# Kernel optimization log

Measured on AMD Instinct MI355X. Metric: run time of the kernel, lower is better.

The kernel has to match this reference:

```python
import jax, jax.numpy as jnp
import numpy as np

EPS = 1e-5

def _conv(x, w, b=None):
    # NCHW conv, stride 1, padding 1 (SAME for 3x3)
    y = jax.lax.conv_general_dilated(x, w, window_strides=(1, 1),
                                     padding=((1, 1), (1, 1)),
                                     dimension_numbers=('NCHW', 'OIHW', 'NCHW'))
    if b is not None:
        y = y + b[None, :, None, None]
    return y


def setup_inputs() -> dict:
    key = jax.random.key(0)
    ks = jax.random.split(key, 8)
    B, H, W = 4, 512, 640
    depth = jax.random.uniform(ks[0], (B, 1, H, W), dtype=jnp.float32) * 100.0
    img_feature = jax.random.normal(ks[1], (B, 16, H, W), dtype=jnp.float32)
    w1 = jax.random.normal(ks[2], (32, 16, 3, 3), dtype=jnp.float32) * 0.05
    b1 = jax.random.normal(ks[3], (32,), dtype=jnp.float32) * 0.05
    gamma = jnp.ones((32,), dtype=jnp.float32)
    beta = jnp.zeros((32,), dtype=jnp.float32)
    rmean = jax.random.normal(ks[4], (32,), dtype=jnp.float32) * 0.05
    rvar = jax.random.uniform(ks[5], (32,), dtype=jnp.float32) + 0.5
    w2 = jax.random.normal(ks[6], (9, 32, 3, 3), dtype=jnp.float32) * 0.05
    return {"depth": depth, "img_feature": img_feature, "w1": w1, "b1": b1,
            "gamma": gamma, "beta": beta, "rmean": rmean, "rvar": rvar, "w2": w2}


def reference(depth, img_feature, w1, b1, gamma, beta, rmean, rvar, w2):
    B, _, H, W = depth.shape
    # depth_propagation_layer: conv -> BN (eval, running stats) -> relu -> conv
    h1 = _conv(img_feature, w1, b1)
    h1 = (h1 - rmean[None, :, None, None]) * (gamma[None, :, None, None]
          * jax.lax.rsqrt(rvar + EPS)[None, :, None, None]) + beta[None, :, None, None]
    h1 = jax.nn.relu(h1)
    logits = _conv(h1, w2)                    # [B, 9, H, W]
    prob = jax.nn.softmax(logits, axis=1)     # per-pixel 3x3 filter weights
    dp = jnp.pad(depth, ((0, 0), (0, 0), (1, 1), (1, 1)), mode='edge')  # [B,1,H+2,W+2]
    patches = jnp.concatenate([dp[:, :, i:i + H, j:j + W]
                               for i in range(3) for j in range(3)], axis=1)  # [B,9,H,W]
    result_depth = jnp.sum(patches * prob, axis=1)  # [B, H, W]
    return result_depth
```

## Files before the change

kernel.cpp:

```cpp
#include <hip/hip_runtime.h>
#include <hip/hip_bf16.h>

#define HH 512
#define WW 640
#define HW (HH*WW)
#define NT 256

typedef short short8  __attribute__((ext_vector_type(8)));
typedef short short4v __attribute__((ext_vector_type(4)));
typedef float f32x16  __attribute__((ext_vector_type(16)));
typedef float f32x4   __attribute__((ext_vector_type(4)));

__device__ inline short f2bf(float f) {
    __hip_bfloat16 h = __float2bfloat16(f);
    short s; __builtin_memcpy(&s, &h, 2);
    return s;
}

__global__ void prep_weights(const float* __restrict__ w1, const float* __restrict__ b1,
                             const float* __restrict__ gamma, const float* __restrict__ beta,
                             const float* __restrict__ rmean, const float* __restrict__ rvar,
                             const float* __restrict__ w2,
                             short* __restrict__ ws_w1, short* __restrict__ ws_w2)
{
    int tid = blockIdx.x*blockDim.x + threadIdx.x;
    int stride = gridDim.x*blockDim.x;
    for (int i = tid; i < 4608; i += stride) {
        int oc = i / 144, rem = i - oc*144, c = rem / 9, t = rem - c*9;
        float a = gamma[oc] * rsqrtf(rvar[oc] + 1e-5f);
        ws_w1[t*512 + oc*16 + c] = f2bf(w1[i] * a);
    }
    for (int i = tid; i < 512; i += stride) {
        int oc = i >> 4, c = i & 15;
        float a = gamma[oc] * rsqrtf(rvar[oc] + 1e-5f);
        float bias = beta[oc] + (b1[oc] - rmean[oc]) * a;
        ws_w1[9*512 + i] = (c == 0) ? f2bf(bias) : (short)0;
    }
    for (int i = tid; i < 4608; i += stride) {
        int t = i >> 9, f = (i >> 5) & 15, c = i & 31;
        float val = (f < 9) ? w2[(f*32 + c)*9 + t] : 0.f;
        ws_w2[i] = f2bf(val);
    }
}

__launch_bounds__(NT, 4)
__global__ void fastprop_main(const float* __restrict__ depth,
                              const float* __restrict__ img,
                              const short* __restrict__ ws_w1,
                              const short* __restrict__ ws_w2,
                              float* __restrict__ out)
{
    __shared__ short s_img[468*16];
    __shared__ short s_h1 [360*32];
    __shared__ float s_depth[340];

    const int tid = threadIdx.x;

    int nid = blockIdx.x;
    int oid = (nid & 7)*640 + (nid >> 3);
    int bz = oid / 1280; int rem = oid - bz*1280;
    int by = rem / 20;   int bx = rem - by*20;
    const int gy0 = by*8, gx0 = bx*32;

    const float* imgb = img   + (size_t)bz*16*HW;
    const float* dpb  = depth + (size_t)bz*HW;

    const int lane = tid & 63;
    const int wid  = tid >> 6;

    const int oc = lane & 31, cg = lane >> 5;
    short8 a1[10];
    #pragma unroll
    for (int t = 0; t < 10; ++t)
        a1[t] = *(const short8*)&ws_w1[t*512 + oc*16 + cg*8];
    short8 bb = (short8)0;
    bb[0] = (cg == 0) ? (short)0x3F80 : (short)0;

    #pragma unroll
    for (int it = 0; it < 2; ++it) {
        int idx = tid + it*NT;
        if (idx < 468) {
            int iy = idx / 36, ix = idx - iy*36;
            int gy = gy0 + iy - 2, gx = gx0 + ix - 2;
            bool v = ((unsigned)gy < HH) && ((unsigned)gx < WW);
            int cy = min(max(gy, 0), HH-1), cx = min(max(gx, 0), WW-1);
            const float* p = imgb + cy*WW + cx;
            float m = v ? 1.f : 0.f;
            short8 v0, v1;
            #pragma unroll
            for (int c = 0; c < 8; ++c)  v0[c] = f2bf(m * p[c*HW]);
            #pragma unroll
            for (int c = 0; c < 8; ++c)  v1[c] = f2bf(m * p[(c+8)*HW]);
            *(short8*)&s_img[idx*16]     = v0;
            *(short8*)&s_img[idx*16 + 8] = v1;
        }
    }
    #pragma unroll
    for (int it = 0; it < 2; ++it) {
        int idx = tid + it*NT;
        if (idx < 340) {
            int ty = idx / 34, tx = idx - ty*34;
            int gy = min(max(gy0 + ty - 1, 0), HH-1);
            int gx = min(max(gx0 + tx - 1, 0), WW-1);
            s_depth[idx] = dpb[gy*WW + gx];
        }
    }
    __syncthreads();

    {
        const int OFS1[9] = {0, 16, 32, 576, 592, 608, 1152, 1168, 1184};

        #pragma unroll
        for (int gi = 0; gi < 3; ++gi) {
            int g    = wid + gi*4;
            int hp   = g*32 + (lane & 31);
            int base = hp*16 + cg*8;
            f32x16 acc;
            #pragma unroll
            for (int i = 0; i < 16; ++i) acc[i] = 0.f;
            acc = __builtin_amdgcn_mfma_f32_32x32x16_bf16(a1[9], bb, acc, 0, 0, 0);
            #pragma unroll
            for (int t = 0; t < 9; ++t)
                acc = __builtin_amdgcn_mfma_f32_32x32x16_bf16(
                         a1[t], *(const short8*)&s_img[base + OFS1[t]], acc, 0, 0, 0);

            if (hp < 360) {
                unsigned hy = (unsigned)hp / 36u;
                int hx = hp - (int)hy*36;
                int gy = gy0 + (int)hy - 1, gx = gx0 + hx - 1;
                bool inb = ((unsigned)gy < HH) && ((unsigned)gx < WW);
                #pragma unroll
                for (int q = 0; q < 4; ++q) {
                    short4v h;
                    #pragma unroll
                    for (int j = 0; j < 4; ++j) {
                        float hv = fmaxf(acc[q*4 + j], 0.f);
                        h[j] = inb ? f2bf(hv) : (short)0;
                    }
                    *(short4v*)&s_h1[hp*32 + 8*q + 4*cg] = h;
                }
            }
        }
    }
    __syncthreads();

    {
        const int fl = lane & 15, cg2 = lane >> 4;
        short8 a2[9];
        #pragma unroll
        for (int t = 0; t < 9; ++t)
            a2[t] = *(const short8*)&ws_w2[t*512 + fl*32 + cg2*8];

        const int OFS2[9] = {-1184, -1152, -1120, -32, 0, 32, 1120, 1152, 1184};

        #pragma unroll
        for (int gi = 0; gi < 4; ++gi) {
            int g  = wid + gi*4;
            int po = g*16 + fl;
            int oy = po >> 5, ox = po & 31;
            int hbase = ((oy + 1)*36 + (ox + 1))*32 + cg2*8;
            f32x4 acc;
            #pragma unroll
            for (int i = 0; i < 4; ++i) acc[i] = 0.f;
            #pragma unroll
            for (int t = 0; t < 9; ++t)
                acc = __builtin_amdgcn_mfma_f32_16x16x32_bf16(
                         a2[t], *(const short8*)&s_h1[hbase + OFS2[t]], acc, 0, 0, 0);

            float num = 0.f, den = 0.f;
            #pragma unroll
            for (int r = 0; r < 4; ++r) {
                int f = cg2*4 + r;
                if (f < 9) {
                    float e = __expf(acc[r]);
                    int fy = f/3, fx = f - fy*3;
                    float d = s_depth[(oy + fy)*34 + (ox + fx)];
                    den += e; num += e * d;
                }
            }
            num += __shfl_xor(num, 16); den += __shfl_xor(den, 16);
            num += __shfl_xor(num, 32); den += __shfl_xor(den, 32);
            if (cg2 == 0)
                out[(size_t)bz*HW + (size_t)(gy0 + oy)*WW + (gx0 + ox)] = num / den;
        }
    }
}

extern "C" void kernel_launch(void* const* d_in, const int* in_sizes, int n_in,
                              void* d_out, int out_size, void* d_ws, size_t ws_size,
                              hipStream_t stream) {
    const float* depth = (const float*)d_in[0];
    const float* img   = (const float*)d_in[1];
    const float* w1    = (const float*)d_in[2];
    const float* b1    = (const float*)d_in[3];
    const float* gamma = (const float*)d_in[4];
    const float* beta  = (const float*)d_in[5];
    const float* rmean = (const float*)d_in[6];
    const float* rvar  = (const float*)d_in[7];
    const float* w2    = (const float*)d_in[8];
    float* out = (float*)d_out;

    short* ws_w1 = (short*)d_ws;
    short* ws_w2 = ws_w1 + 5120;

    prep_weights<<<16, NT, 0, stream>>>(w1, b1, gamma, beta, rmean, rvar, w2,
                                        ws_w1, ws_w2);
    fastprop_main<<<5120, NT, 0, stream>>>(depth, img, ws_w1, ws_w2, out);
}
```

Before: 64.05 us.

## Switch LDS tiles to channel-planar layout and reuse h1 rows across output rows

Shared-memory image and h1 tiles move from pixel-interleaved to channel-group planar layout with padded planes, aiming to cut LDS bank conflicts on the MFMA operand loads. The image staging loop is split into half-channel work items so each thread issues fewer loads per iteration. In the second conv, each wave now handles two adjacent output rows and loads four h1 rows once into registers, feeding both accumulators and cutting redundant LDS reads. This raises register pressure per wave, which could hurt occupancy.

```diff
diff --git a/kernel.cpp b/kernel.cpp
--- a/kernel.cpp
+++ b/kernel.cpp
@@ -5,6 +5,8 @@
 #define WW 640
 #define HW (HH*WW)
 #define NT 256
+#define IMPLANEP (468*8 + 8)
+#define H1PLANEP (360*8 + 8)
 
 typedef short short8  __attribute__((ext_vector_type(8)));
 typedef short short4v __attribute__((ext_vector_type(4)));
@@ -50,8 +52,8 @@
                               const short* __restrict__ ws_w2,
                               float* __restrict__ out)
 {
-    __shared__ short s_img[468*16];
-    __shared__ short s_h1 [360*32];
+    __shared__ short s_img[2*IMPLANEP];
+    __shared__ short s_h1 [4*H1PLANEP];
     __shared__ float s_depth[340];
 
     const int tid = threadIdx.x;
@@ -76,24 +78,18 @@
     short8 bb = (short8)0;
     bb[0] = (cg == 0) ? (short)0x3F80 : (short)0;
 
-    #pragma unroll
-    for (int it = 0; it < 2; ++it) {
-        int idx = tid + it*NT;
-        if (idx < 468) {
-            int iy = idx / 36, ix = idx - iy*36;
-            int gy = gy0 + iy - 2, gx = gx0 + ix - 2;
-            bool v = ((unsigned)gy < HH) && ((unsigned)gx < WW);
-            int cy = min(max(gy, 0), HH-1), cx = min(max(gx, 0), WW-1);
-            const float* p = imgb + cy*WW + cx;
-            float m = v ? 1.f : 0.f;
-            short8 v0, v1;
-            #pragma unroll
-            for (int c = 0; c < 8; ++c)  v0[c] = f2bf(m * p[c*HW]);
-            #pragma unroll
-            for (int c = 0; c < 8; ++c)  v1[c] = f2bf(m * p[(c+8)*HW]);
-            *(short8*)&s_img[idx*16]     = v0;
-            *(short8*)&s_img[idx*16 + 8] = v1;
-        }
+    for (int g = tid; g < 936; g += NT) {
+        int pixel = g >> 1, half = g & 1;
+        int iy = pixel / 36, ix = pixel - iy*36;
+        int gy = gy0 + iy - 2, gx = gx0 + ix - 2;
+        bool v = ((unsigned)gy < HH) && ((unsigned)gx < WW);
+        int cy = min(max(gy, 0), HH-1), cx = min(max(gx, 0), WW-1);
+        const float* p = imgb + (size_t)(half*8)*HW + cy*WW + cx;
+        float m = v ? 1.f : 0.f;
+        short8 vv;
+        #pragma unroll
+        for (int c = 0; c < 8; ++c) vv[c] = f2bf(m * p[c*HW]);
+        *(short8*)&s_img[half*IMPLANEP + pixel*8] = vv;
     }
     #pragma unroll
     for (int it = 0; it < 2; ++it) {
@@ -108,13 +104,14 @@
     __syncthreads();
 
     {
-        const int OFS1[9] = {0, 16, 32, 576, 592, 608, 1152, 1168, 1184};
+        const int OFS1[9] = {0, 8, 16, 288, 296, 304, 576, 584, 592};
+        const int px = lane & 31;
 
         #pragma unroll
         for (int gi = 0; gi < 3; ++gi) {
             int g    = wid + gi*4;
-            int hp   = g*32 + (lane & 31);
-            int base = hp*16 + cg*8;
+            int hp   = g*32 + px;
+            int base = cg*IMPLANEP + hp*8;
             f32x16 acc;
             #pragma unroll
             for (int i = 0; i < 16; ++i) acc[i] = 0.f;
@@ -137,7 +134,7 @@
                         float hv = fmaxf(acc[q*4 + j], 0.f);
                         h[j] = inb ? f2bf(hv) : (short)0;
                     }
-                    *(short4v*)&s_h1[hp*32 + 8*q + 4*cg] = h;
+                    *(short4v*)&s_h1[q*H1PLANEP + hp*8 + 4*cg] = h;
                 }
             }
         }
@@ -151,37 +148,59 @@
         for (int t = 0; t < 9; ++t)
             a2[t] = *(const short8*)&ws_w2[t*512 + fl*32 + cg2*8];
 
-        const int OFS2[9] = {-1184, -1152, -1120, -32, 0, 32, 1120, 1152, 1184};
-
-        #pragma unroll
-        for (int gi = 0; gi < 4; ++gi) {
-            int g  = wid + gi*4;
-            int po = g*16 + fl;
-            int oy = po >> 5, ox = po & 31;
-            int hbase = ((oy + 1)*36 + (ox + 1))*32 + cg2*8;
-            f32x4 acc;
-            #pragma unroll
-            for (int i = 0; i < 4; ++i) acc[i] = 0.f;
-            #pragma unroll
-            for (int t = 0; t < 9; ++t)
-                acc = __builtin_amdgcn_mfma_f32_16x16x32_bf16(
-                         a2[t], *(const short8*)&s_h1[hbase + OFS2[t]], acc, 0, 0, 0);
-
-            float num = 0.f, den = 0.f;
-            #pragma unroll
-            for (int r = 0; r < 4; ++r) {
-                int f = cg2*4 + r;
-                if (f < 9) {
-                    float e = __expf(acc[r]);
-                    int fy = f/3, fx = f - fy*3;
-                    float d = s_depth[(oy + fy)*34 + (ox + fx)];
-                    den += e; num += e * d;
+        const int r0 = 2*wid;
+
+        #pragma unroll
+        for (int chh = 0; chh < 2; ++chh) {
+            const int ox0 = chh*16;
+            const int colbase = cg2*H1PLANEP + (ox0 + fl)*8;
+
+            short8 F[4][3];
+            #pragma unroll
+            for (int i = 0; i < 3; ++i)
+                #pragma unroll
+                for (int dx = 0; dx < 3; ++dx)
+                    F[i][dx] = *(const short8*)&s_h1[colbase + ((r0 + i)*36 + dx)*8];
+            #pragma unroll
+            for (int dx = 0; dx < 3; ++dx)
+                F[3][dx] = *(const short8*)&s_h1[colbase + ((r0 + 3)*36 + dx)*8];
+
+            f32x4 acc0, acc1;
+            #pragma unroll
+            for (int i = 0; i < 4; ++i) { acc0[i] = 0.f; acc1[i] = 0.f; }
+            #pragma unroll
+            for (int ty = 0; ty < 3; ++ty)
+                #pragma unroll
+                for (int tx = 0; tx < 3; ++tx)
+                    acc0 = __builtin_amdgcn_mfma_f32_16x16x32_bf16(
+                             a2[ty*3 + tx], F[ty][tx], acc0, 0, 0, 0);
+            #pragma unroll
+            for (int ty = 0; ty < 3; ++ty)
+                #pragma unroll
+                for (int tx = 0; tx < 3; ++tx)
+                    acc1 = __builtin_amdgcn_mfma_f32_16x16x32_bf16(
+                             a2[ty*3 + tx], F[ty + 1][tx], acc1, 0, 0, 0);
+
+            #pragma unroll
+            for (int rr = 0; rr < 2; ++rr) {
+                f32x4 lg = rr ? acc1 : acc0;
+                int oy = r0 + rr, ox = ox0 + fl;
+                float num = 0.f, den = 0.f;
+                #pragma unroll
+                for (int r = 0; r < 4; ++r) {
+                    int f = cg2*4 + r;
+                    if (f < 9) {
+                        float e = __expf(lg[r]);
+                        int fy = f/3, fx = f - fy*3;
+                        float d = s_depth[(oy + fy)*34 + (ox + fx)];
+                        den += e; num += e * d;
+                    }
                 }
+                num += __shfl_xor(num, 16); den += __shfl_xor(den, 16);
+                num += __shfl_xor(num, 32); den += __shfl_xor(den, 32);
+                if (cg2 == 0)
+                    out[(size_t)bz*HW + (size_t)(gy0 + oy)*WW + (gx0 + ox)] = num / den;
             }
-            num += __shfl_xor(num, 16); den += __shfl_xor(den, 16);
-            num += __shfl_xor(num, 32); den += __shfl_xor(den, 32);
-            if (cg2 == 0)
-                out[(size_t)bz*HW + (size_t)(gy0 + oy)*WW + (gx0 + ox)] = num / den;
         }
     }
 }
```

After: 63.41 us. About the same (-1.0%).

## Split LDS tiles into channel planes and double threads per block

Applied to the files above, without the earlier changes.

Stores the image tile and the intermediate h1 tile in LDS as separate 8-channel planes with padding, instead of interleaving all channels per pixel. The conv offsets and fragment addressing are rewritten to match, which is meant to reduce LDS bank conflicts on the MFMA operand loads. The block grows from 256 to 512 threads with a higher launch-bounds occupancy target, so each wave does fewer tile groups. Risks: the tighter register budget may cause spilling, and the first conv stage splits 12 groups unevenly across 8 waves.

```diff
diff --git a/kernel.cpp b/kernel.cpp
--- a/kernel.cpp
+++ b/kernel.cpp
@@ -4,7 +4,9 @@
 #define HH 512
 #define WW 640
 #define HW (HH*WW)
-#define NT 256
+#define NT 512
+#define IMPLANEP (432*8 + 8)
+#define H1PLANEP (360*8 + 8)
 
 typedef short short8  __attribute__((ext_vector_type(8)));
 typedef short short4v __attribute__((ext_vector_type(4)));
@@ -43,15 +45,15 @@
     }
 }
 
-__launch_bounds__(NT, 4)
+__launch_bounds__(NT, 8)
 __global__ void fastprop_main(const float* __restrict__ depth,
                               const float* __restrict__ img,
                               const short* __restrict__ ws_w1,
                               const short* __restrict__ ws_w2,
                               float* __restrict__ out)
 {
-    __shared__ short s_img[468*16];
-    __shared__ short s_h1 [360*32];
+    __shared__ short s_img[2*IMPLANEP];
+    __shared__ short s_h1 [4*H1PLANEP];
     __shared__ float s_depth[340];
 
     const int tid = threadIdx.x;
@@ -68,53 +70,42 @@
     const int lane = tid & 63;
     const int wid  = tid >> 6;
 
-    const int oc = lane & 31, cg = lane >> 5;
-    short8 a1[10];
-    #pragma unroll
-    for (int t = 0; t < 10; ++t)
-        a1[t] = *(const short8*)&ws_w1[t*512 + oc*16 + cg*8];
-    short8 bb = (short8)0;
-    bb[0] = (cg == 0) ? (short)0x3F80 : (short)0;
-
-    #pragma unroll
-    for (int it = 0; it < 2; ++it) {
-        int idx = tid + it*NT;
-        if (idx < 468) {
-            int iy = idx / 36, ix = idx - iy*36;
-            int gy = gy0 + iy - 2, gx = gx0 + ix - 2;
-            bool v = ((unsigned)gy < HH) && ((unsigned)gx < WW);
-            int cy = min(max(gy, 0), HH-1), cx = min(max(gx, 0), WW-1);
-            const float* p = imgb + cy*WW + cx;
-            float m = v ? 1.f : 0.f;
-            short8 v0, v1;
-            #pragma unroll
-            for (int c = 0; c < 8; ++c)  v0[c] = f2bf(m * p[c*HW]);
-            #pragma unroll
-            for (int c = 0; c < 8; ++c)  v1[c] = f2bf(m * p[(c+8)*HW]);
-            *(short8*)&s_img[idx*16]     = v0;
-            *(short8*)&s_img[idx*16 + 8] = v1;
-        }
+    for (int g = tid; g < 864; g += NT) {
+        int pixel = g >> 1, half = g & 1;
+        int iy = pixel / 36, ix = pixel - iy*36;
+        int gy = gy0 + iy - 2, gx = gx0 + ix - 2;
+        bool v = ((unsigned)gy < HH) && ((unsigned)gx < WW);
+        int cy = min(max(gy, 0), HH-1), cx = min(max(gx, 0), WW-1);
+        const float* p = imgb + (size_t)(half*8)*HW + cy*WW + cx;
+        float m = v ? 1.f : 0.f;
+        short8 vv;
+        #pragma unroll
+        for (int c = 0; c < 8; ++c) vv[c] = f2bf(m * p[c*HW]);
+        *(short8*)&s_img[half*IMPLANEP + pixel*8] = vv;
     }
-    #pragma unroll
-    for (int it = 0; it < 2; ++it) {
-        int idx = tid + it*NT;
-        if (idx < 340) {
-            int ty = idx / 34, tx = idx - ty*34;
-            int gy = min(max(gy0 + ty - 1, 0), HH-1);
-            int gx = min(max(gx0 + tx - 1, 0), WW-1);
-            s_depth[idx] = dpb[gy*WW + gx];
-        }
+    if (tid < 340) {
+        int ty = tid / 34, tx = tid - ty*34;
+        int gy = min(max(gy0 + ty - 1, 0), HH-1);
+        int gx = min(max(gx0 + tx - 1, 0), WW-1);
+        s_depth[tid] = dpb[gy*WW + gx];
     }
     __syncthreads();
 
     {
-        const int OFS1[9] = {0, 16, 32, 576, 592, 608, 1152, 1168, 1184};
+        const int oc = lane & 31, cg = lane >> 5;
+        short8 a1[10];
+        #pragma unroll
+        for (int t = 0; t < 10; ++t)
+            a1[t] = *(const short8*)&ws_w1[t*512 + oc*16 + cg*8];
+        short8 bb = (short8)0;
+        bb[0] = (cg == 0) ? (short)0x3F80 : (short)0;
 
-        #pragma unroll
-        for (int gi = 0; gi < 3; ++gi) {
-            int g    = wid + gi*4;
-            int hp   = g*32 + (lane & 31);
-            int base = hp*16 + cg*8;
+        const int OFS1[9] = {0, 8, 16, 288, 296, 304, 576, 584, 592};
+        const int px = lane & 31;
+
+        for (int g = wid; g < 12; g += 8) {
+            int hp   = g*32 + px;
+            int base = cg*IMPLANEP + hp*8;
             f32x16 acc;
             #pragma unroll
             for (int i = 0; i < 16; ++i) acc[i] = 0.f;
@@ -137,7 +128,7 @@
                         float hv = fmaxf(acc[q*4 + j], 0.f);
                         h[j] = inb ? f2bf(hv) : (short)0;
                     }
-                    *(short4v*)&s_h1[hp*32 + 8*q + 4*cg] = h;
+                    *(short4v*)&s_h1[q*H1PLANEP + hp*8 + 4*cg] = h;
                 }
             }
         }
@@ -151,14 +142,12 @@
         for (int t = 0; t < 9; ++t)
             a2[t] = *(const short8*)&ws_w2[t*512 + fl*32 + cg2*8];
 
-        const int OFS2[9] = {-1184, -1152, -1120, -32, 0, 32, 1120, 1152, 1184};
+        const int OFS2[9] = {-296, -288, -280, -8, 0, 8, 280, 288, 296};
 
-        #pragma unroll
-        for (int gi = 0; gi < 4; ++gi) {
-            int g  = wid + gi*4;
+        for (int g = wid; g < 16; g += 8) {
             int po = g*16 + fl;
             int oy = po >> 5, ox = po & 31;
-            int hbase = ((oy + 1)*36 + (ox + 1))*32 + cg2*8;
+            int hbase = cg2*H1PLANEP + ((oy + 1)*36 + (ox + 1))*8;
             f32x4 acc;
             #pragma unroll
             for (int i = 0; i < 4; ++i) acc[i] = 0.f;
@@ -203,7 +192,7 @@
     short* ws_w1 = (short*)d_ws;
     short* ws_w2 = ws_w1 + 5120;
 
-    prep_weights<<<16, NT, 0, stream>>>(w1, b1, gamma, beta, rmean, rvar, w2,
-                                        ws_w1, ws_w2);
+    prep_weights<<<16, 256, 0, stream>>>(w1, b1, gamma, beta, rmean, rvar, w2,
+                                         ws_w1, ws_w2);
     fastprop_main<<<5120, NT, 0, stream>>>(depth, img, ws_w1, ws_w2, out);
 }
```

Result: slower. 99.09 us (+54.7%).
